# Optimization experiments

Measured on AMD Instinct MI355X. Metric: run time of the kernel, lower is better.

Reference implementation:

```python
import jax, jax.numpy as jnp
import numpy as np

BATCH, SEQ_LEN, HIDDEN, N_TYPES = 8, 1024, 256, 4
MAX_SPAN = 12


def _span_indices(seq_len: int, max_span_length: int):
    # Enumerate (start, end) pairs in the exact order of the original triple loop:
    # start ascending, end ascending within [start, min(start+max_span, seq_len)).
    starts, ends = [], []
    for s in range(seq_len):
        for e in range(s, min(s + max_span_length, seq_len)):
            starts.append(s)
            ends.append(e)
    return np.asarray(starts, np.int32), np.asarray(ends, np.int32)


def setup_inputs() -> dict:
    key = jax.random.key(0)
    k1, k2, k3 = jax.random.split(key, 3)
    hidden_states = jax.random.normal(k1, (BATCH, SEQ_LEN, HIDDEN), dtype=jnp.float32)
    # Stacked nn.Linear(2H -> H) weights for each entity type: W[t] has shape [H, 2H]
    W = jax.random.normal(k2, (N_TYPES, HIDDEN, 2 * HIDDEN), dtype=jnp.float32) * 0.02
    b = jax.random.normal(k3, (N_TYPES, HIDDEN), dtype=jnp.float32) * 0.02
    return {"hidden_states": hidden_states, "W": W, "b": b, "max_span_length": MAX_SPAN}


def reference(hidden_states, W, b, max_span_length):
    B, S, H = hidden_states.shape
    T = W.shape[0]
    start_idx, end_idx = _span_indices(S, int(max_span_length))  # [N]
    N = start_idx.shape[0]
    h_start = hidden_states[:, start_idx, :]          # [B, N, H]
    h_end = hidden_states[:, end_idx, :]              # [B, N, H]
    cat = jnp.concatenate([h_start, h_end], axis=-1)  # [B, N, 2H]
    # Per-type linear: y = x @ W_t^T + b_t, entity type is the innermost stacking axis
    out = jnp.einsum('bnc,thc->bnth', cat, W) + b     # [B, N, T, H]
    return out.reshape(B, N * T, H)
```

## Files before the change

### kernel.cpp

```cpp
#include <hip/hip_runtime.h>
#include <hip/hip_bf16.h>
#include <cstdint>
#include <cstddef>

#define BATCH   8
#define SEQLEN  1024
#define HIDDEN  256
#define NTYPES  4
#define NSPAN   12222
#define NFULL   12156
#define NPAD    12288
#define KDIM    512
#define NCOL    1024

typedef __bf16 bf16x8 __attribute__((ext_vector_type(8)));
typedef float  f32x4  __attribute__((ext_vector_type(4)));

#define AS1 __attribute__((address_space(1)))
#define AS3 __attribute__((address_space(3)))

__device__ __forceinline__ void load16(const __bf16* g, __bf16* l) {
    __builtin_amdgcn_global_load_lds((AS1 const void*)g, (AS3 void*)l, 16, 0, 0);
}

__global__ void cvt_bf16(const float* __restrict__ src, __bf16* __restrict__ dst, int n) {
    int i = (blockIdx.x * 256 + threadIdx.x) * 4;
    if (i + 3 < n) {
        float4 f = *(const float4*)(src + i);
        struct alignas(8) B4 { __bf16 a, b, c, d; };
        B4 v;
        v.a = (__bf16)f.x; v.b = (__bf16)f.y; v.c = (__bf16)f.z; v.d = (__bf16)f.w;
        *(B4*)(dst + i) = v;
    }
}

__global__ void mk_idx(int* __restrict__ sA, int* __restrict__ eA) {
    int n = blockIdx.x * 256 + threadIdx.x;
    if (n >= NPAD) return;
    int s = 0, e = 0;
    if (n < NFULL) {
        s = n / 12;
        e = s + (n - s * 12);
    } else if (n < NSPAN) {
        int r = n - NFULL;
        s = SEQLEN - 11;
        int cnt = 11;
        while (r >= cnt) { r -= cnt; --cnt; ++s; }
        e = s + r;
    }
    sA[n] = s; eA[n] = e;
}

__global__ __launch_bounds__(256) void span_gemm(
    const __bf16* __restrict__ Hbf,
    const __bf16* __restrict__ Wbf,
    const int*    __restrict__ idxS,
    const int*    __restrict__ idxE,
    const float*  __restrict__ bias,
    float*        __restrict__ out)
{
    __shared__ alignas(16) __bf16 As[128 * 32];
    __shared__ alignas(16) __bf16 Bs[128 * 32];

    const int tid  = threadIdx.x;
    const int wave = tid >> 6;
    const int lane = tid & 63;
    const int wm   = (wave >> 1) * 64;
    const int wn   = (wave & 1) * 64;
    const int lr   = lane & 15;
    const int lq   = lane >> 4;

    const int j0 = blockIdx.x * 128;
    const int n0 = blockIdx.y * 128;
    const int b  = blockIdx.z;

    const int l0  = wave * 1024 + lane * 8;
    const int l1  = l0 + 512;
    const int mm0 = l0 >> 5, kk0 = l0 & 31;
    const int mm1 = l1 >> 5, kk1 = l1 & 31;

    const int s0 = idxS[n0 + mm0], e0 = idxE[n0 + mm0];
    const int s1 = idxS[n0 + mm1], e1 = idxE[n0 + mm1];

    const __bf16* hb = Hbf + (size_t)b * (SEQLEN * HIDDEN);
    const __bf16* w0 = Wbf + (size_t)(j0 + mm0) * KDIM + kk0;
    const __bf16* w1 = Wbf + (size_t)(j0 + mm1) * KDIM + kk1;

    f32x4 acc[4][4];
#pragma unroll
    for (int i = 0; i < 4; ++i)
#pragma unroll
        for (int j = 0; j < 4; ++j)
            acc[i][j] = (f32x4){0.f, 0.f, 0.f, 0.f};

    for (int half = 0; half < 2; ++half) {
        const __bf16* a0  = hb + (half ? e0 : s0) * HIDDEN + kk0;
        const __bf16* a1  = hb + (half ? e1 : s1) * HIDDEN + kk1;
        const __bf16* wb0 = w0 + half * HIDDEN;
        const __bf16* wb1 = w1 + half * HIDDEN;

        for (int ks = 0; ks < 8; ++ks) {
            const int c0 = ks * 32;
            __syncthreads();
            load16(a0  + c0, &As[l0]);
            load16(a1  + c0, &As[l1]);
            load16(wb0 + c0, &Bs[l0]);
            load16(wb1 + c0, &Bs[l1]);
            __syncthreads();

            bf16x8 af[4], bfv[4];
#pragma unroll
            for (int mi = 0; mi < 4; ++mi)
                af[mi] = *(const bf16x8*)(As + (wm + mi * 16 + lr) * 32 + lq * 8);
#pragma unroll
            for (int ni = 0; ni < 4; ++ni)
                bfv[ni] = *(const bf16x8*)(Bs + (wn + ni * 16 + lr) * 32 + lq * 8);
#pragma unroll
            for (int mi = 0; mi < 4; ++mi)
#pragma unroll
                for (int ni = 0; ni < 4; ++ni)
                    acc[mi][ni] = __builtin_amdgcn_mfma_f32_16x16x32_bf16(
                        af[mi], bfv[ni], acc[mi][ni], 0, 0, 0);
        }
    }

    float bv[4];
#pragma unroll
    for (int ni = 0; ni < 4; ++ni) bv[ni] = bias[j0 + wn + ni * 16 + lr];

    const size_t obase = (size_t)b * NSPAN * NCOL;
#pragma unroll
    for (int mi = 0; mi < 4; ++mi) {
#pragma unroll
        for (int r = 0; r < 4; ++r) {
            const int n = n0 + wm + mi * 16 + lq * 4 + r;
            if (n < NSPAN) {
                float* op = out + obase + (size_t)n * NCOL + (j0 + wn + lr);
#pragma unroll
                for (int ni = 0; ni < 4; ++ni)
                    op[ni * 16] = acc[mi][ni][r] + bv[ni];
            }
        }
    }
}

extern "C" void kernel_launch(void* const* d_in, const int* in_sizes, int n_in,
                              void* d_out, int out_size, void* d_ws, size_t ws_size,
                              hipStream_t stream) {
    const float* hid  = (const float*)d_in[0];
    const float* W    = (const float*)d_in[1];
    const float* bias = (const float*)d_in[2];
    float* out = (float*)d_out;

    char* ws = (char*)d_ws;
    __bf16* Wbf = (__bf16*)ws;
    __bf16* Hbf = (__bf16*)(ws + (size_t)1048576);
    int* idxS = (int*)(ws + (size_t)(1048576 + 4194304));
    int* idxE = idxS + NPAD;

    cvt_bf16<<<512,  256, 0, stream>>>(W,   Wbf, NCOL * KDIM);
    cvt_bf16<<<2048, 256, 0, stream>>>(hid, Hbf, BATCH * SEQLEN * HIDDEN);
    mk_idx<<<NPAD / 256, 256, 0, stream>>>(idxS, idxE);
    span_gemm<<<dim3(8, 96, BATCH), 256, 0, stream>>>(Hbf, Wbf, idxS, idxE, bias, out);
}
```

Baseline: 454.3 us.

## Factor span projection into per-token GEMM plus broadcast-add epilogue

Splits the concat-linear into separate start and end projections. A single GEMM over the 8192 tokens produces a 2048-column table P holding the start half and end half of W for every token. An epilogue kernel then builds each span row as P_start[s] + P_end[e] + bias and writes it out. This cuts the MFMA work by about 12x, because the per-span GEMM recomputed the same projections for every span. In exchange it adds a large intermediate buffer (fp32, or bf16 if workspace is short) and an extra kernel, and the output write of about 400MB stays the dominant cost.

```diff
diff --git a/kernel.cpp b/kernel.cpp
--- a/kernel.cpp
+++ b/kernel.cpp
@@ -12,6 +12,8 @@
 #define NPAD    12288
 #define KDIM    512
 #define NCOL    1024
+#define MROWS   8192
+#define PCOLS   2048
 
 typedef __bf16 bf16x8 __attribute__((ext_vector_type(8)));
 typedef float  f32x4  __attribute__((ext_vector_type(4)));
@@ -31,6 +33,131 @@
         B4 v;
         v.a = (__bf16)f.x; v.b = (__bf16)f.y; v.c = (__bf16)f.z; v.d = (__bf16)f.w;
         *(B4*)(dst + i) = v;
+    }
+}
+
+__global__ void mk_wbf2(const float* __restrict__ W, __bf16* __restrict__ dst) {
+    int idx = (blockIdx.x * 256 + threadIdx.x) * 4;
+    int jp = idx >> 8, k = idx & 255;
+    int t = (jp & 1023) >> 8, h = jp & 255;
+    int c = k + ((jp >> 10) << 8);
+    float4 f = *(const float4*)(W + ((size_t)(t * 256 + h)) * 512 + c);
+    struct alignas(8) B4 { __bf16 a, b, c, d; };
+    B4 v;
+    v.a = (__bf16)f.x; v.b = (__bf16)f.y; v.c = (__bf16)f.z; v.d = (__bf16)f.w;
+    *(B4*)(dst + idx) = v;
+}
+
+template <typename PT>
+__global__ __launch_bounds__(256) void pgemm(
+    const __bf16* __restrict__ Hbf,
+    const __bf16* __restrict__ Wbf2,
+    PT*           __restrict__ P)
+{
+    __shared__ alignas(16) __bf16 As[128 * 32];
+    __shared__ alignas(16) __bf16 Bs[128 * 32];
+
+    const int tid  = threadIdx.x;
+    const int wave = tid >> 6;
+    const int lane = tid & 63;
+    const int wm   = (wave >> 1) * 64;
+    const int wn   = (wave & 1) * 64;
+    const int lr   = lane & 15;
+    const int lq   = lane >> 4;
+
+    const int j0 = blockIdx.x * 128;
+    const int m0 = blockIdx.y * 128;
+
+    const int l0  = wave * 1024 + lane * 8;
+    const int l1  = l0 + 512;
+    const int mm0 = l0 >> 5, kk0 = l0 & 31;
+    const int mm1 = l1 >> 5, kk1 = l1 & 31;
+
+    const __bf16* a0 = Hbf  + (size_t)(m0 + mm0) * HIDDEN + kk0;
+    const __bf16* a1 = Hbf  + (size_t)(m0 + mm1) * HIDDEN + kk1;
+    const __bf16* w0 = Wbf2 + (size_t)(j0 + mm0) * HIDDEN + kk0;
+    const __bf16* w1 = Wbf2 + (size_t)(j0 + mm1) * HIDDEN + kk1;
+
+    f32x4 acc[4][4];
+#pragma unroll
+    for (int i = 0; i < 4; ++i)
+#pragma unroll
+        for (int j = 0; j < 4; ++j)
+            acc[i][j] = (f32x4){0.f, 0.f, 0.f, 0.f};
+
+    for (int ks = 0; ks < 8; ++ks) {
+        const int c0 = ks * 32;
+        __syncthreads();
+        load16(a0 + c0, &As[l0]);
+        load16(a1 + c0, &As[l1]);
+        load16(w0 + c0, &Bs[l0]);
+        load16(w1 + c0, &Bs[l1]);
+        __syncthreads();
+
+        bf16x8 af[4], bfv[4];
+#pragma unroll
+        for (int mi = 0; mi < 4; ++mi)
+            af[mi] = *(const bf16x8*)(As + (wm + mi * 16 + lr) * 32 + lq * 8);
+#pragma unroll
+        for (int ni = 0; ni < 4; ++ni)
+            bfv[ni] = *(const bf16x8*)(Bs + (wn + ni * 16 + lr) * 32 + lq * 8);
+#pragma unroll
+        for (int mi = 0; mi < 4; ++mi)
+#pragma unroll
+            for (int ni = 0; ni < 4; ++ni)
+                acc[mi][ni] = __builtin_amdgcn_mfma_f32_16x16x32_bf16(
+                    af[mi], bfv[ni], acc[mi][ni], 0, 0, 0);
+    }
+
+#pragma unroll
+    for (int mi = 0; mi < 4; ++mi) {
+#pragma unroll
+        for (int r = 0; r < 4; ++r) {
+            const int m = m0 + wm + mi * 16 + lq * 4 + r;
+            PT* op = P + (size_t)m * PCOLS + (j0 + wn + lr);
+#pragma unroll
+            for (int ni = 0; ni < 4; ++ni)
+                op[ni * 16] = (PT)acc[mi][ni][r];
+        }
+    }
+}
+
+template <typename PT>
+__device__ __forceinline__ f32x4 ld4(const PT* p) {
+    if constexpr (sizeof(PT) == 4) {
+        return *(const f32x4*)p;
+    } else {
+        struct alignas(8) B4 { __bf16 a, b, c, d; };
+        B4 v = *(const B4*)p;
+        return (f32x4){(float)v.a, (float)v.b, (float)v.c, (float)v.d};
+    }
+}
+
+template <typename PT>
+__global__ __launch_bounds__(256) void span_epi(
+    const PT*    __restrict__ P,
+    const float* __restrict__ bias,
+    float*       __restrict__ out)
+{
+    const int bx = blockIdx.x;
+    const int b  = blockIdx.y;
+    const int s  = (bx & 7) * 128 + (bx >> 3);
+    const int j  = threadIdx.x * 4;
+
+    const size_t prow = (size_t)(b * SEQLEN + s) * PCOLS;
+    f32x4 ps = ld4(P + prow + j);
+    const f32x4 bv = *(const f32x4*)(bias + j);
+    ps += bv;
+
+    int len; long nbase;
+    if (s <= SEQLEN - 12) { len = 12; nbase = (long)s * 12; }
+    else { len = SEQLEN - s; nbase = NFULL + (long)(1036 - s) * (s - 1013) / 2; }
+
+    float*    ob = out + ((size_t)b * NSPAN + nbase) * NCOL + j;
+    const PT* pe = P + prow + NCOL + j;
+    for (int k = 0; k < len; ++k) {
+        f32x4 o = ps + ld4(pe + (size_t)k * PCOLS);
+        *(f32x4*)(ob + (size_t)k * NCOL) = o;
     }
 }
 
@@ -153,13 +280,29 @@
     float* out = (float*)d_out;
 
     char* ws = (char*)d_ws;
-    __bf16* Wbf = (__bf16*)ws;
+    __bf16* Wb  = (__bf16*)ws;
     __bf16* Hbf = (__bf16*)(ws + (size_t)1048576);
-    int* idxS = (int*)(ws + (size_t)(1048576 + 4194304));
-    int* idxE = idxS + NPAD;
-
-    cvt_bf16<<<512,  256, 0, stream>>>(W,   Wbf, NCOL * KDIM);
+    const size_t base  = (size_t)1048576 + 4194304;
+    const size_t needF = base + (size_t)MROWS * PCOLS * sizeof(float);
+    const size_t needH = base + (size_t)MROWS * PCOLS * sizeof(__bf16);
+
     cvt_bf16<<<2048, 256, 0, stream>>>(hid, Hbf, BATCH * SEQLEN * HIDDEN);
-    mk_idx<<<NPAD / 256, 256, 0, stream>>>(idxS, idxE);
-    span_gemm<<<dim3(8, 96, BATCH), 256, 0, stream>>>(Hbf, Wbf, idxS, idxE, bias, out);
-}
+
+    if (ws_size >= needF) {
+        float* P = (float*)(ws + base);
+        mk_wbf2<<<512, 256, 0, stream>>>(W, Wb);
+        pgemm<float><<<dim3(PCOLS / 128, MROWS / 128), 256, 0, stream>>>(Hbf, Wb, P);
+        span_epi<float><<<dim3(SEQLEN, BATCH), 256, 0, stream>>>(P, bias, out);
+    } else if (ws_size >= needH) {
+        __bf16* P = (__bf16*)(ws + base);
+        mk_wbf2<<<512, 256, 0, stream>>>(W, Wb);
+        pgemm<__bf16><<<dim3(PCOLS / 128, MROWS / 128), 256, 0, stream>>>(Hbf, Wb, P);
+        span_epi<__bf16><<<dim3(SEQLEN, BATCH), 256, 0, stream>>>(P, bias, out);
+    } else {
+        int* idxS = (int*)(ws + base);
+        int* idxE = idxS + NPAD;
+        cvt_bf16<<<512, 256, 0, stream>>>(W, Wb, NCOL * KDIM);
+        mk_idx<<<NPAD / 256, 256, 0, stream>>>(idxS, idxE);
+        span_gemm<<<dim3(8, 96, BATCH), 256, 0, stream>>>(Hbf, Wb, idxS, idxE, bias, out);
+    }
+}
```

Result: no change. 452.7 us (-0.4%).
